# Performance work log

Hardware: AMD Instinct MI355X
Metric: run time of the kernel (lower is better)

## Reference

```python
import jax, jax.numpy as jnp
import numpy as np

N_HEADS = 16
D_EMBD = 1024
D_HEAD = D_EMBD // N_HEADS  # 64


def setup_inputs() -> dict:
    key = jax.random.key(0)
    k0, k1, k2, k3, k4 = jax.random.split(key, 5)
    s = 1.0 / np.sqrt(D_EMBD)
    return {
        "x": jax.random.normal(k0, (4, 2048, D_EMBD), dtype=jnp.float32),
        "w_in": jax.random.normal(k1, (D_EMBD, 3 * D_EMBD), dtype=jnp.float32) * s,
        "b_in": jax.random.normal(k2, (3 * D_EMBD,), dtype=jnp.float32) * 0.02,
        "w_out": jax.random.normal(k3, (D_EMBD, D_EMBD), dtype=jnp.float32) * s,
        "b_out": jax.random.normal(k4, (D_EMBD,), dtype=jnp.float32) * 0.02,
    }


def reference(x, w_in, b_in, w_out, b_out):
    B, S, D = x.shape
    # fused QKV projection; torch .chunk(3) order in source is k, q, v
    kqv = x @ w_in + b_in                      # [B, S, 3D]
    k, q, v = jnp.split(kqv, 3, axis=-1)
    # split heads: [B, S, D] -> [B, H, S, Dh]
    def heads(t):
        return t.reshape(B, S, N_HEADS, D_HEAD).transpose(0, 2, 1, 3)
    q, k, v = heads(q), heads(k), heads(v)
    # attention scores, explicit O(S^2) matrix (naive, unmasked path)
    scores = jnp.einsum("bhsd,bhtd->bhst", q, k) / jnp.sqrt(
        jnp.asarray(D_HEAD, dtype=x.dtype)
    )
    probs = jax.nn.softmax(scores, axis=-1)    # [B, H, S, S]
    out = jnp.einsum("bhst,bhtd->bhsd", probs, v)
    out = out.transpose(0, 2, 1, 3).reshape(B, S, D)
    return out @ w_out + b_out
```

## Files before the change

kernel.cpp:

```cpp
#include <hip/hip_runtime.h>

typedef unsigned short u16;
typedef __attribute__((ext_vector_type(8))) short bf16x8;
typedef __attribute__((ext_vector_type(4))) float f32x4;

#define MFMA(a, b, c) __builtin_amdgcn_mfma_f32_16x16x32_bf16(a, b, c, 0, 0, 0)

#if defined(__has_builtin)
#if __has_builtin(__builtin_amdgcn_exp2f)
#define EXP2(x) __builtin_amdgcn_exp2f(x)
#endif
#endif
#ifndef EXP2
#define EXP2(x) exp2f(x)
#endif

#define ASYNC16(g, l)                                                      \
  __builtin_amdgcn_global_load_lds(                                        \
      (const __attribute__((address_space(1))) void*)(g),                  \
      (__attribute__((address_space(3))) void*)(l), 16, 0, 0)

__device__ __forceinline__ u16 f2bf(float x) {
  union { float f; unsigned u; } v; v.f = x;
  unsigned r = (v.u + 0x7fffu + ((v.u >> 16) & 1u)) >> 16;
  return (u16)r;
}

__device__ __forceinline__ unsigned pack_bf2(float a, float b) {
  unsigned ua = __float_as_uint(a) + 0x8000u;
  unsigned ub = __float_as_uint(b) + 0x8000u;
  return __builtin_amdgcn_perm(ub, ua, 0x07060302u);
}

__device__ __forceinline__ bf16x8 exp_pack8(const f32x4 a, const f32x4 b) {
  union { unsigned u[4]; bf16x8 v; } r;
  r.u[0] = pack_bf2(EXP2(a[0]), EXP2(a[1]));
  r.u[1] = pack_bf2(EXP2(a[2]), EXP2(a[3]));
  r.u[2] = pack_bf2(EXP2(b[0]), EXP2(b[1]));
  r.u[3] = pack_bf2(EXP2(b[2]), EXP2(b[3]));
  return r.v;
}

__global__ __launch_bounds__(256) void prep_fused(const float* __restrict__ w_in,
                                                  u16* __restrict__ wT_in,
                                                  const float* __restrict__ w_out,
                                                  u16* __restrict__ wT_out,
                                                  const float4* __restrict__ x,
                                                  uint2* __restrict__ xb) {
  int bid = blockIdx.x;
  int tid = threadIdx.x;
  if (bid >= 4096) {
    int idx = (bid - 4096) * 256 + tid;
    float4 v = x[idx];
    xb[idx] = make_uint2(pack_bf2(v.x, v.y), pack_bf2(v.z, v.w));
    return;
  }
  const float* in;
  u16* out;
  int R = 1024, C, bx, by;
  if (bid < 3072) {
    in = w_in; out = wT_in; C = 3072; bx = bid % 96; by = bid / 96;
  } else {
    int b2 = bid - 3072;
    in = w_out; out = wT_out; C = 1024; bx = b2 & 31; by = b2 >> 5;
  }
  __shared__ float tile[32][33];
  int tx = tid & 31, ty = tid >> 5;
  int c0 = bx * 32, r0 = by * 32;
#pragma unroll
  for (int i = 0; i < 32; i += 8)
    tile[ty + i][tx] = in[(size_t)(r0 + ty + i) * C + c0 + tx];
  __syncthreads();
#pragma unroll
  for (int i = 0; i < 32; i += 8)
    out[(size_t)(c0 + ty + i) * R + r0 + tx] = f2bf(tile[tx][ty + i]);
}

#define BM 128
#define BN 128
#define BK 64

template <int OUT_F32, int NBX>
__global__ __launch_bounds__(256, 2) void gemm_bt(const u16* __restrict__ A,
                                                  const u16* __restrict__ Bt,
                                                  const float* __restrict__ bias,
                                                  void* __restrict__ Cout,
                                                  int M, int N, int K, int ldc,
                                                  int sc_lo, int sc_hi, float qs) {
  __shared__ __align__(16) u16 As[BM * BK];
  __shared__ __align__(16) u16 Bs[BN * BK];
  int id = blockIdx.x;
  int cpx = gridDim.x >> 3;
  int swz = (id & 7) * cpx + (id >> 3);
  int bn = (swz % NBX) * BN, bm = (swz / NBX) * BM;
  int tid = threadIdx.x;
  int wave = tid >> 6, lane = tid & 63;
  int quad = lane >> 4, l16 = lane & 15;
  int wm = (wave >> 1) * 64, wn = (wave & 1) * 64;

  f32x4 acc[4][4] = {};

  int lrow = lane >> 3, lcol = (lane & 7) * 8;
  const u16* gA = A + (size_t)(bm + wave * 8 + lrow) * K + lcol;
  const u16* gB = Bt + (size_t)(bn + wave * 8 + lrow) * K + lcol;
  u16* lA = &As[wave * 8 * BK];
  u16* lB = &Bs[wave * 8 * BK];

  for (int k0 = 0; k0 < K; k0 += BK) {
#pragma unroll
    for (int p = 0; p < 4; ++p) {
      ASYNC16(gA + (size_t)p * 32 * K, lA + p * 32 * BK);
      ASYNC16(gB + (size_t)p * 32 * K, lB + p * 32 * BK);
    }
    gA += BK;
    gB += BK;
    __syncthreads();
#pragma unroll
    for (int kk = 0; kk < BK; kk += 32) {
      bf16x8 af[4], bfr[4];
#pragma unroll
      for (int i = 0; i < 4; ++i)
        af[i] = *(const bf16x8*)&As[(wm + 16 * i + l16) * BK + kk + quad * 8];
#pragma unroll
      for (int j = 0; j < 4; ++j)
        bfr[j] = *(const bf16x8*)&Bs[(wn + 16 * j + l16) * BK + kk + quad * 8];
#pragma unroll
      for (int i = 0; i < 4; ++i)
#pragma unroll
        for (int j = 0; j < 4; ++j)
          acc[i][j] = MFMA(af[i], bfr[j], acc[i][j]);
    }
    __syncthreads();
  }

#pragma unroll
  for (int i = 0; i < 4; ++i) {
#pragma unroll
    for (int j = 0; j < 4; ++j) {
      int gn = bn + wn + 16 * j + l16;
      float bv = bias[gn];
      float sc = (gn >= sc_lo && gn < sc_hi) ? qs : 1.0f;
#pragma unroll
      for (int r = 0; r < 4; ++r) {
        int gm = bm + wm + 16 * i + quad * 4 + r;
        float v = (acc[i][j][r] + bv) * sc;
        if (OUT_F32)
          ((float*)Cout)[(size_t)gm * ldc + gn] = v;
        else
          ((u16*)Cout)[(size_t)gm * ldc + gn] = f2bf(v);
      }
    }
  }
}

#define SEQ 2048
#define ROWS3 3072

__global__ void v_transpose(const u16* __restrict__ kqv, u16* __restrict__ vt) {
  int bh = blockIdx.y;
  int b = bh >> 4, h = bh & 15;
  int t0 = blockIdx.x * 64;
  int tid = threadIdx.x;
  __shared__ u16 tile[64][72];
  int r = tid >> 3, c = (tid & 7) * 8;
#pragma unroll
  for (int p = 0; p < 2; ++p)
    *(uint4*)&tile[p * 32 + r][c] =
        *(const uint4*)&kqv[(size_t)b * SEQ * ROWS3 + (size_t)(t0 + p * 32 + r) * ROWS3 +
                            2048 + h * 64 + c];
  __syncthreads();
#pragma unroll
  for (int p = 0; p < 2; ++p) {
    int d = p * 32 + r;
    u16 tmp[8];
#pragma unroll
    for (int i = 0; i < 8; ++i) {
      int pos = c + i;
      int k = 16 * (2 * (pos >> 5) + ((pos >> 2) & 1)) + ((pos >> 3) & 3) * 4 + (pos & 3);
      tmp[i] = tile[k][d];
    }
    *(uint4*)&vt[(size_t)bh * 64 * SEQ + (size_t)d * SEQ + t0 + c] = *(uint4*)tmp;
  }
}

__global__ __launch_bounds__(256, 4) void attn_kernel(const u16* __restrict__ kqv,
                                                      const u16* __restrict__ vt,
                                                      u16* __restrict__ out) {
  int g = blockIdx.x;
  int bh = g & 63, qtile = g >> 6;
  int b = bh >> 4, h = bh & 15;
  int tid = threadIdx.x, wave = tid >> 6, lane = tid & 63;
  int quad = lane >> 4, l16 = lane & 15;

  __shared__ __align__(16) u16 Ks[2][64 * 64];
  __shared__ __align__(16) u16 Vts[3][64 * 64];

  const u16* base = kqv + (size_t)b * SEQ * ROWS3;
  int hcol = h * 64;
  const u16* vbase = vt + (size_t)bh * 64 * SEQ;

  bf16x8 qf[2][2];
#pragma unroll
  for (int t = 0; t < 2; ++t) {
    int s = qtile * 128 + wave * 32 + t * 16 + l16;
    const u16* qrow = base + (size_t)s * ROWS3 + 1024 + hcol;
    qf[t][0] = *(const bf16x8*)(qrow + quad * 8);
    qf[t][1] = *(const bf16x8*)(qrow + 32 + quad * 8);
  }

  bf16x8 ones;
#pragma unroll
  for (int i = 0; i < 8; ++i) ones[i] = (short)0x3F80;

  f32x4 o[2][4] = {};
  f32x4 ol[2] = {};
  const f32x4 zf = {};

  int prow = lane & 7;
  int pchk = (lane >> 3) * 8;

  int rb2 = (l16 >> 3) * 512;
  int r8 = (l16 & 7) * 8;

  const u16* kg = base + hcol + (size_t)(wave * 16 + prow) * ROWS3 + pchk;
  const u16* vg = vbase + (size_t)(wave * 16 + prow) * SEQ + pchk;

#define STAGE_K(bi)                                      \
  do {                                                   \
    ASYNC16(kg, &Ks[bi][wave * 16 * 64]);                \
    ASYNC16(kg + (size_t)8 * ROWS3, &Ks[bi][(wave * 16 + 8) * 64]); \
    kg += (size_t)64 * ROWS3;                            \
  } while (0)
#define STAGE_V(bi)                                      \
  do {                                                   \
    ASYNC16(vg, &Vts[bi][wave * 16 * 64]);               \
    ASYNC16(vg + (size_t)8 * SEQ, &Vts[bi][(wave * 16 + 8) * 64]); \
    vg += 64;                                            \
  } while (0)

  const int NT = SEQ / 64;

  STAGE_K(0);
  STAGE_V(0);
  __syncthreads();
  STAGE_K(1);
  STAGE_V(1);

  bf16x8 pa00, pa01, pa10, pa11;
  {
    const u16* ks = &Ks[0][0];
    f32x4 s0[4], s1[4];
#pragma unroll
    for (int j = 0; j < 4; ++j) {
      bf16x8 k0 = *(const bf16x8*)&ks[j * 1024 + rb2 + quad * 64 + r8];
      bf16x8 k1 = *(const bf16x8*)&ks[j * 1024 + rb2 + 256 + quad * 64 + r8];
      s0[j] = MFMA(k0, qf[0][0], zf);
      s0[j] = MFMA(k1, qf[0][1], s0[j]);
      s1[j] = MFMA(k0, qf[1][0], zf);
      s1[j] = MFMA(k1, qf[1][1], s1[j]);
    }
    pa00 = exp_pack8(s0[0], s0[1]);
    pa01 = exp_pack8(s0[2], s0[3]);
    pa10 = exp_pack8(s1[0], s1[1]);
    pa11 = exp_pack8(s1[2], s1[3]);
  }

  int v_rd = 0;
  int v_st = 2;

  for (int t = 0; t < NT - 1; ++t) {
    __syncthreads();

    if (t + 2 < NT) {
      STAGE_K(t & 1);
      STAGE_V(v_st);
    }

    const u16* ks = &Ks[(t + 1) & 1][0];
    const u16* vs = &Vts[v_rd][0];

    __builtin_amdgcn_s_setprio(1);

    f32x4 s0[4], s1[4];
#pragma unroll
    for (int j = 0; j < 4; ++j) {
      bf16x8 k0 = *(const bf16x8*)&ks[j * 1024 + rb2 + quad * 64 + r8];
      bf16x8 k1 = *(const bf16x8*)&ks[j * 1024 + rb2 + 256 + quad * 64 + r8];
      s0[j] = MFMA(k0, qf[0][0], zf);
      s0[j] = MFMA(k1, qf[0][1], s0[j]);
      s1[j] = MFMA(k0, qf[1][0], zf);
      s1[j] = MFMA(k1, qf[1][1], s1[j]);
    }

    bf16x8 pn00 = exp_pack8(s0[0], s0[1]);
    bf16x8 pn01 = exp_pack8(s0[2], s0[3]);
    bf16x8 pn10 = exp_pack8(s1[0], s1[1]);
    bf16x8 pn11 = exp_pack8(s1[2], s1[3]);

#pragma unroll
    for (int d = 0; d < 4; ++d) {
      bf16x8 v0 = *(const bf16x8*)&vs[d * 1024 + rb2 + quad * 64 + r8];
      bf16x8 v1 = *(const bf16x8*)&vs[d * 1024 + rb2 + 256 + quad * 64 + r8];
      o[0][d] = MFMA(pa00, v0, o[0][d]);
      o[0][d] = MFMA(pa01, v1, o[0][d]);
      o[1][d] = MFMA(pa10, v0, o[1][d]);
      o[1][d] = MFMA(pa11, v1, o[1][d]);
    }
    ol[0] = MFMA(pa00, ones, ol[0]);
    ol[0] = MFMA(pa01, ones, ol[0]);
    ol[1] = MFMA(pa10, ones, ol[1]);
    ol[1] = MFMA(pa11, ones, ol[1]);

    __builtin_amdgcn_s_setprio(0);

    pa00 = pn00; pa01 = pn01; pa10 = pn10; pa11 = pn11;
    v_rd = (v_rd == 2) ? 0 : v_rd + 1;
    v_st = (v_st == 2) ? 0 : v_st + 1;
  }

  __syncthreads();
  {
    const u16* vs = &Vts[v_rd][0];
    __builtin_amdgcn_s_setprio(1);
#pragma unroll
    for (int d = 0; d < 4; ++d) {
      bf16x8 v0 = *(const bf16x8*)&vs[d * 1024 + rb2 + quad * 64 + r8];
      bf16x8 v1 = *(const bf16x8*)&vs[d * 1024 + rb2 + 256 + quad * 64 + r8];
      o[0][d] = MFMA(pa00, v0, o[0][d]);
      o[0][d] = MFMA(pa01, v1, o[0][d]);
      o[1][d] = MFMA(pa10, v0, o[1][d]);
      o[1][d] = MFMA(pa11, v1, o[1][d]);
    }
    ol[0] = MFMA(pa00, ones, ol[0]);
    ol[0] = MFMA(pa01, ones, ol[0]);
    ol[1] = MFMA(pa10, ones, ol[1]);
    ol[1] = MFMA(pa11, ones, ol[1]);
    __builtin_amdgcn_s_setprio(0);
  }

#pragma unroll
  for (int t = 0; t < 2; ++t)
#pragma unroll
    for (int r = 0; r < 4; ++r) {
      float inv = 1.0f / ol[t][r];
      int s = qtile * 128 + wave * 32 + t * 16 + quad * 4 + r;
      u16* orow = out + (size_t)(b * SEQ + s) * 1024 + hcol;
#pragma unroll
      for (int d = 0; d < 4; ++d) orow[16 * d + l16] = f2bf(o[t][d][r] * inv);
    }
#undef STAGE_K
#undef STAGE_V
}

extern "C" void kernel_launch(void* const* d_in, const int* in_sizes, int n_in,
                              void* d_out, int out_size, void* d_ws, size_t ws_size,
                              hipStream_t stream) {
  const float* x     = (const float*)d_in[0];
  const float* w_in  = (const float*)d_in[1];
  const float* b_in  = (const float*)d_in[2];
  const float* w_out = (const float*)d_in[3];
  const float* b_out = (const float*)d_in[4];
  float* outp = (float*)d_out;

  char* p = (char*)d_ws;
  u16* wT_in  = (u16*)p; p += (size_t)3072 * 1024 * 2;
  u16* wT_out = (u16*)p; p += (size_t)1024 * 1024 * 2;
  u16* xb     = (u16*)p; p += (size_t)8192 * 1024 * 2;
  u16* kqv    = (u16*)p; p += (size_t)8192 * 3072 * 2;
  u16* attn   = (u16*)p;
  u16* vtbuf  = xb;

  prep_fused<<<dim3(12288), dim3(256), 0, stream>>>(
      w_in, wT_in, w_out, wT_out, (const float4*)x, (uint2*)xb);

  const float QSCALE = 0.125f * 1.44269504088896f;
  gemm_bt<0, 3072 / BN><<<dim3((3072 / BN) * (8192 / BM)), 256, 0, stream>>>(
      xb, wT_in, b_in, (void*)kqv, 8192, 3072, 1024, 3072, 1024, 2048, QSCALE);

  v_transpose<<<dim3(SEQ / 64, 64), 256, 0, stream>>>(kqv, vtbuf);

  attn_kernel<<<dim3(1024), 256, 0, stream>>>(kqv, vtbuf, attn);

  gemm_bt<1, 1024 / BN><<<dim3((1024 / BN) * (8192 / BM)), 256, 0, stream>>>(
      attn, wT_out, b_out, (void*)outp, 8192, 1024, 1024, 1024, 0, 0, 1.0f);
}
```

Before: 280.0 us.

## Fuse V transpose into QKV GEMM epilogue, drop separate transpose kernel

The QKV projection GEMM now handles the V columns (bn >= 2048) in its epilogue. It stages the tile in shared memory and writes V directly in the transposed, permuted layout the attention kernel expects. K and Q go to a narrower 2048-wide buffer. This removes a kernel launch and a round trip of V through global memory, at the cost of extra shared memory (a 128x132 tile) in the GEMM, which may reduce occupancy.

New measurement: 286.0 us. 2.1% more time.

```diff
diff --git a/kernel.cpp b/kernel.cpp
--- a/kernel.cpp
+++ b/kernel.cpp
@@ -19,6 +19,9 @@
   __builtin_amdgcn_global_load_lds(                                        \
       (const __attribute__((address_space(1))) void*)(g),                  \
       (__attribute__((address_space(3))) void*)(l), 16, 0, 0)
+
+#define SEQ 2048
+#define KQW 2048
 
 __device__ __forceinline__ u16 f2bf(float x) {
   union { float f; unsigned u; } v; v.f = x;
@@ -80,11 +83,12 @@
 #define BN 128
 #define BK 64
 
-template <int OUT_F32, int NBX>
+template <int MODE, int NBX>
 __global__ __launch_bounds__(256, 2) void gemm_bt(const u16* __restrict__ A,
                                                   const u16* __restrict__ Bt,
                                                   const float* __restrict__ bias,
                                                   void* __restrict__ Cout,
+                                                  u16* __restrict__ vtout,
                                                   int M, int N, int K, int ldc,
                                                   int sc_lo, int sc_hi, float qs) {
   __shared__ __align__(16) u16 As[BM * BK];
@@ -133,6 +137,41 @@
     __syncthreads();
   }
 
+  if constexpr (MODE == 2) {
+    if (bn >= 2048) {
+      __shared__ u16 vtile[128][132];
+#pragma unroll
+      for (int j = 0; j < 4; ++j) {
+        int vc = wn + 16 * j + l16;
+        float bv = bias[bn + vc];
+#pragma unroll
+        for (int i = 0; i < 4; ++i)
+#pragma unroll
+          for (int r = 0; r < 4; ++r)
+            vtile[vc][wm + 16 * i + quad * 4 + r] = f2bf(acc[i][j][r] + bv);
+      }
+      __syncthreads();
+      int vc = tid >> 1, tt = tid & 1;
+      int d = vc & 63;
+      int b = bm >> 11, s0 = bm & 2047;
+      int bh = b * 16 + ((bn - 2048) >> 6) + (vc >> 6);
+      u16* row = vtout + (size_t)bh * 64 * SEQ + (size_t)d * SEQ + s0 + tt * 64;
+#pragma unroll
+      for (int c8 = 0; c8 < 8; ++c8) {
+        u16 tmp[8];
+#pragma unroll
+        for (int e = 0; e < 8; ++e) {
+          int pos = c8 * 8 + e;
+          int k = 16 * (2 * (pos >> 5) + ((pos >> 2) & 1)) + ((pos >> 3) & 3) * 4 +
+                  (pos & 3);
+          tmp[e] = vtile[vc][tt * 64 + k];
+        }
+        *(uint4*)&row[c8 * 8] = *(uint4*)tmp;
+      }
+      return;
+    }
+  }
+
 #pragma unroll
   for (int i = 0; i < 4; ++i) {
 #pragma unroll
@@ -144,42 +183,12 @@
       for (int r = 0; r < 4; ++r) {
         int gm = bm + wm + 16 * i + quad * 4 + r;
         float v = (acc[i][j][r] + bv) * sc;
-        if (OUT_F32)
+        if (MODE == 1)
           ((float*)Cout)[(size_t)gm * ldc + gn] = v;
         else
           ((u16*)Cout)[(size_t)gm * ldc + gn] = f2bf(v);
       }
     }
-  }
-}
-
-#define SEQ 2048
-#define ROWS3 3072
-
-__global__ void v_transpose(const u16* __restrict__ kqv, u16* __restrict__ vt) {
-  int bh = blockIdx.y;
-  int b = bh >> 4, h = bh & 15;
-  int t0 = blockIdx.x * 64;
-  int tid = threadIdx.x;
-  __shared__ u16 tile[64][72];
-  int r = tid >> 3, c = (tid & 7) * 8;
-#pragma unroll
-  for (int p = 0; p < 2; ++p)
-    *(uint4*)&tile[p * 32 + r][c] =
-        *(const uint4*)&kqv[(size_t)b * SEQ * ROWS3 + (size_t)(t0 + p * 32 + r) * ROWS3 +
-                            2048 + h * 64 + c];
-  __syncthreads();
-#pragma unroll
-  for (int p = 0; p < 2; ++p) {
-    int d = p * 32 + r;
-    u16 tmp[8];
-#pragma unroll
-    for (int i = 0; i < 8; ++i) {
-      int pos = c + i;
-      int k = 16 * (2 * (pos >> 5) + ((pos >> 2) & 1)) + ((pos >> 3) & 3) * 4 + (pos & 3);
-      tmp[i] = tile[k][d];
-    }
-    *(uint4*)&vt[(size_t)bh * 64 * SEQ + (size_t)d * SEQ + t0 + c] = *(uint4*)tmp;
   }
 }
 
@@ -195,7 +204,7 @@
   __shared__ __align__(16) u16 Ks[2][64 * 64];
   __shared__ __align__(16) u16 Vts[3][64 * 64];
 
-  const u16* base = kqv + (size_t)b * SEQ * ROWS3;
+  const u16* base = kqv + (size_t)b * SEQ * KQW;
   int hcol = h * 64;
   const u16* vbase = vt + (size_t)bh * 64 * SEQ;
 
@@ -203,7 +212,7 @@
 #pragma unroll
   for (int t = 0; t < 2; ++t) {
     int s = qtile * 128 + wave * 32 + t * 16 + l16;
-    const u16* qrow = base + (size_t)s * ROWS3 + 1024 + hcol;
+    const u16* qrow = base + (size_t)s * KQW + 1024 + hcol;
     qf[t][0] = *(const bf16x8*)(qrow + quad * 8);
     qf[t][1] = *(const bf16x8*)(qrow + 32 + quad * 8);
   }
@@ -222,14 +231,14 @@
   int rb2 = (l16 >> 3) * 512;
   int r8 = (l16 & 7) * 8;
 
-  const u16* kg = base + hcol + (size_t)(wave * 16 + prow) * ROWS3 + pchk;
+  const u16* kg = base + hcol + (size_t)(wave * 16 + prow) * KQW + pchk;
   const u16* vg = vbase + (size_t)(wave * 16 + prow) * SEQ + pchk;
 
 #define STAGE_K(bi)                                      \
   do {                                                   \
     ASYNC16(kg, &Ks[bi][wave * 16 * 64]);                \
-    ASYNC16(kg + (size_t)8 * ROWS3, &Ks[bi][(wave * 16 + 8) * 64]); \
-    kg += (size_t)64 * ROWS3;                            \
+    ASYNC16(kg + (size_t)8 * KQW, &Ks[bi][(wave * 16 + 8) * 64]); \
+    kg += (size_t)64 * KQW;                              \
   } while (0)
 #define STAGE_V(bi)                                      \
   do {                                                   \
@@ -366,21 +375,19 @@
   u16* wT_in  = (u16*)p; p += (size_t)3072 * 1024 * 2;
   u16* wT_out = (u16*)p; p += (size_t)1024 * 1024 * 2;
   u16* xb     = (u16*)p; p += (size_t)8192 * 1024 * 2;
-  u16* kqv    = (u16*)p; p += (size_t)8192 * 3072 * 2;
+  u16* kqv    = (u16*)p; p += (size_t)8192 * 2048 * 2;
+  u16* vtbuf  = (u16*)p; p += (size_t)64 * 64 * 2048 * 2;
   u16* attn   = (u16*)p;
-  u16* vtbuf  = xb;
 
   prep_fused<<<dim3(12288), dim3(256), 0, stream>>>(
       w_in, wT_in, w_out, wT_out, (const float4*)x, (uint2*)xb);
 
   const float QSCALE = 0.125f * 1.44269504088896f;
-  gemm_bt<0, 3072 / BN><<<dim3((3072 / BN) * (8192 / BM)), 256, 0, stream>>>(
-      xb, wT_in, b_in, (void*)kqv, 8192, 3072, 1024, 3072, 1024, 2048, QSCALE);
-
-  v_transpose<<<dim3(SEQ / 64, 64), 256, 0, stream>>>(kqv, vtbuf);
+  gemm_bt<2, 3072 / BN><<<dim3((3072 / BN) * (8192 / BM)), 256, 0, stream>>>(
+      xb, wT_in, b_in, (void*)kqv, vtbuf, 8192, 3072, 1024, 2048, 1024, 2048, QSCALE);
 
   attn_kernel<<<dim3(1024), 256, 0, stream>>>(kqv, vtbuf, attn);
 
   gemm_bt<1, 1024 / BN><<<dim3((1024 / BN) * (8192 / BM)), 256, 0, stream>>>(
-      attn, wT_out, b_out, (void*)outp, 8192, 1024, 1024, 1024, 0, 0, 1.0f);
-}
+      attn, wT_out, b_out, (void*)outp, nullptr, 8192, 1024, 1024, 1024, 0, 0, 1.0f);
+}
```
